# Kernel tuning notes

Measured on AMD Instinct MI355X. Metric: run time of the kernel, lower is better.

The kernel has to match this reference:

```python
import jax, jax.numpy as jnp
import numpy as np

# Fixed production-scale dims (equal-size graphs -> no ragged padding needed)
B, NPG, C, H, L, FFN, NC = 16, 512, 128, 8, 4, 512, 4
D = C // H          # head dim = 16
T = NPG + 1         # +1 virtual graph token
EPG = 8192          # edges per graph (avg degree 16)
E = B * EPG


def _ln(x, g, b, eps=1e-5):
    m = x.mean(-1, keepdims=True)
    v = ((x - m) ** 2).mean(-1, keepdims=True)
    return (x - m) * jax.lax.rsqrt(v + eps) * g + b


def setup_inputs() -> dict:
    key = jax.random.key(0)
    ks = jax.random.split(key, 24)
    N = B * NPG
    node_feats = jax.random.normal(ks[0], (N, 3), jnp.float32)
    # intra-graph edges: local endpoints + per-graph node offset (matches batch_ptr math)
    local = jax.random.randint(ks[1], (2, B, EPG), 0, NPG)
    offs = (jnp.arange(B) * NPG)[None, :, None]
    edge_index = (local + offs).reshape(2, E)
    edge_attr = jax.random.randint(ks[2], (E,), 0, 10)

    def nrm(k, shape, scale=0.02):
        return jax.random.normal(k, shape, jnp.float32) * scale

    params = {
        "W_node": nrm(ks[3], (3, C), 0.3), "b_node": jnp.zeros((C,), jnp.float32),
        "graph_token": nrm(ks[4], (C,), 1.0),
        "edge_bias_table": nrm(ks[5], (11, H), 0.1).at[0].set(0.0),  # padding_idx=0
        "in_deg_emb": nrm(ks[6], (512, C)).at[0].set(0.0),           # padding_idx=0
        "out_deg_emb": nrm(ks[7], (512, C)).at[0].set(0.0),
        "vnode_bias": nrm(ks[8], (H,), 1.0),
        "Wq": nrm(ks[9], (L, C, C)), "bq": jnp.zeros((L, C), jnp.float32),
        "Wk": nrm(ks[10], (L, C, C)), "bk": jnp.zeros((L, C), jnp.float32),
        "Wv": nrm(ks[11], (L, C, C)), "bv": jnp.zeros((L, C), jnp.float32),
        "Wo": nrm(ks[12], (L, C, C)), "bo": jnp.zeros((L, C), jnp.float32),
        "ln1_g": jnp.ones((L, C), jnp.float32), "ln1_b": jnp.zeros((L, C), jnp.float32),
        "ln2_g": jnp.ones((L, C), jnp.float32), "ln2_b": jnp.zeros((L, C), jnp.float32),
        "W1": nrm(ks[13], (L, C, FFN)), "b1": jnp.zeros((L, FFN), jnp.float32),
        "W2": nrm(ks[14], (L, FFN, C)), "b2": jnp.zeros((L, C), jnp.float32),
        "normf_g": jnp.ones((C,), jnp.float32), "normf_b": jnp.zeros((C,), jnp.float32),
        "Wc1": nrm(ks[15], (C, C // 2)), "bc1": jnp.zeros((C // 2,), jnp.float32),
        "Wc2": nrm(ks[16], (C // 2, NC)), "bc2": jnp.zeros((NC,), jnp.float32),
    }
    return {"node_feats": node_feats, "edge_index": edge_index,
            "edge_attr": edge_attr, "num_graphs": B, **params}


def reference(node_feats, W_node, b_node, graph_token, edge_bias_table,
              in_deg_emb, out_deg_emb, vnode_bias,
              Wq, bq, Wk, bk, Wv, bv, Wo, bo,
              ln1_g, ln1_b, ln2_g, ln2_b, W1, b1, W2, b2,
              normf_g, normf_b, Wc1, bc1, Wc2, bc2,
              edge_index, edge_attr, num_graphs):
    N = node_feats.shape[0]
    npg = N // num_graphs
    t = npg + 1
    src, dst = edge_index[0], edge_index[1]
    # degree encoders (scatter_add of ones == segment_sum)
    in_deg = jnp.clip(jax.ops.segment_sum(jnp.ones_like(dst), dst, num_segments=N), 0, 511)
    out_deg = jnp.clip(jax.ops.segment_sum(jnp.ones_like(src), src, num_segments=N), 0, 511)
    x_enc = node_feats @ W_node + b_node + in_deg_emb[in_deg] + out_deg_emb[out_deg]
    # equal-size graphs with sorted batch ids -> padding loop is a reshape, mask all-False
    x = jnp.concatenate(
        [jnp.broadcast_to(graph_token, (num_graphs, 1, C)),
         x_enc.reshape(num_graphs, npg, C)], axis=1)  # [B, T, C]
    # attention bias: vnode row/col + scattered edge-attr embeddings
    bias = jnp.zeros((num_graphs, H, t, t), jnp.float32)
    bias = bias.at[:, :, 0, :].set(vnode_bias[None, :, None])
    bias = bias.at[:, :, :, 0].set(vnode_bias[None, :, None])
    eb = edge_bias_table[jnp.clip(edge_attr, 0, 9) + 1]  # [E, H]
    g = src // npg
    sl = src - g * npg + 1
    dl = dst - g * npg + 1
    bias = bias.at[g, :, sl, dl].add(eb)  # duplicate edges accumulate (scatter_add)
    scale = 1.0 / np.sqrt(D).astype(np.float32)
    for l in range(L):  # key_padding_mask is all-False here -> masked_fill is a no-op
        h = _ln(x, ln1_g[l], ln1_b[l])
        q = (h @ Wq[l] + bq[l]).reshape(num_graphs, t, H, D)
        k = (h @ Wk[l] + bk[l]).reshape(num_graphs, t, H, D)
        v = (h @ Wv[l] + bv[l]).reshape(num_graphs, t, H, D)
        scores = jnp.einsum('bthd,bshd->bhts', q, k) * scale + bias
        attn = jax.nn.softmax(scores, axis=-1)
        o = jnp.einsum('bhts,bshd->bthd', attn, v).reshape(num_graphs, t, C)
        x = x + o @ Wo[l] + bo[l]
        h2 = _ln(x, ln2_g[l], ln2_b[l])
        x = x + jax.nn.gelu(h2 @ W1[l] + b1[l], approximate=False) @ W2[l] + b2[l]
    x = _ln(x, normf_g, normf_b)
    gr = x[:, 0, :]  # virtual-node readout
    return jax.nn.gelu(gr @ Wc1 + bc1, approximate=False) @ Wc2 + bc2
```

## Files before the change

kernel.cpp:

```cpp
#include <hip/hip_runtime.h>
#include <hip/hip_bf16.h>

#define BB 16
#define NPG 512
#define CC 128
#define HH 8
#define LL 4
#define FFN 512
#define NCLS 4
#define DD 16
#define TT 513
#define EE 131072
#define NNODES 8192
#define ROWS (BB * TT)
#define ECAP 64
#define SP 544
#define ESTR 68

static constexpr size_t XROWS = (size_t)BB * TT;
static constexpr size_t XSZ   = XROWS * CC;
static constexpr size_t VTSZ  = (size_t)BB * HH * DD * SP;

typedef unsigned short ushort_t;
typedef __attribute__((ext_vector_type(8))) short short8;
typedef __attribute__((ext_vector_type(4))) float floatx4;

__device__ __forceinline__ float gelu_exact(float v) {
    return 0.5f * v * (1.0f + erff(v * 0.70710678118654752440f));
}
__device__ __forceinline__ ushort_t f2bf(float f) {
    union { float f; unsigned u; } c; c.f = f;
    unsigned u = c.u;
    return (ushort_t)((u + 0x7FFFu + ((u >> 16) & 1u)) >> 16);
}
__device__ __forceinline__ int swz(int row, int col, int stride) {
    int kb = col >> 3;
    return row * stride + (((kb ^ (row & 7)) << 3) | (col & 7));
}

__device__ __forceinline__ void qkv_stage8(const ushort_t* hs,
                                           const ushort_t* Wtq, const float* bq_,
                                           const ushort_t* Wtk, const float* bk_,
                                           const ushort_t* Wtv, const float* bv_,
                                           ushort_t* qb, ushort_t* kb, ushort_t* vt,
                                           int b, int t0, int wave, int lq, int quad) {
    const short* hsS = (const short*)hs;
    int c = wave * 16 + lq;
    const short* Ws[3] = {(const short*)Wtq, (const short*)Wtk, (const short*)Wtv};
    const float* bs[3] = {bq_, bk_, bv_};
    size_t rB = (size_t)c * CC;

    #pragma unroll
    for (int m = 0; m < 3; ++m) {
        const short* W = Ws[m];
        floatx4 a0 = {0.f,0.f,0.f,0.f};
        #pragma unroll
        for (int k0 = 0; k0 < CC; k0 += 32) {
            short8 af = *(const short8*)(hsS + swz(lq, k0 + quad * 8, 128));
            short8 b0 = *(const short8*)(W + rB + k0 + quad * 8);
            a0 = __builtin_amdgcn_mfma_f32_16x16x32_bf16(af, b0, a0, 0, 0, 0);
        }
        float bv0 = bs[m][c];
        #pragma unroll
        for (int rg = 0; rg < 4; ++rg) {
            int t = t0 + quad * 4 + rg;
            if (t >= TT) continue;
            size_t r = (size_t)b * TT + t;
            float v0 = a0[rg] + bv0;
            if (m == 0) {
                qb[r * CC + c] = f2bf(v0 * 0.25f);
            } else if (m == 1) {
                kb[r * CC + c] = f2bf(v0);
            } else {
                vt[((size_t)(b * HH + wave) * DD + lq) * SP + t] = f2bf(v0);
            }
        }
    }
}

__global__ __launch_bounds__(256) void deg_csr_tr_kernel(const int* __restrict__ ei,
                                                         const int* __restrict__ ea,
                                                         int* __restrict__ deg_in,
                                                         int* __restrict__ deg_out,
                                                         int* __restrict__ cnt,
                                                         int* __restrict__ ebuf,
                                                         const float* __restrict__ Wq,
                                                         const float* __restrict__ Wk,
                                                         const float* __restrict__ Wv,
                                                         const float* __restrict__ Wo,
                                                         const float* __restrict__ W1,
                                                         const float* __restrict__ W2,
                                                         ushort_t* __restrict__ wtqkvo,
                                                         ushort_t* __restrict__ wt1,
                                                         ushort_t* __restrict__ wt2) {
    int bid = blockIdx.x;
    int tid = threadIdx.x;
    if (bid < 512) {
        int e = bid * 256 + tid;
        int src = ei[e], dst = ei[EE + e];
        atomicAdd(&deg_out[src], 1);
        atomicAdd(&deg_in[dst], 1);
        int g = src >> 9;
        int sl = src - (g << 9) + 1;
        int dl = dst - (g << 9) + 1;
        int a = ea[e];
        a = (a < 0) ? 0 : (a > 9 ? 9 : a);
        a += 1;
        int row = g * TT + sl;
        int pos = atomicAdd(&cnt[row], 1);
        if (pos < ECAP) ebuf[(size_t)row * ECAP + pos] = dl | (a << 16);
        return;
    }
    int z = bid - 512;
    const float* src; ushort_t* dst; int K, N, tile;
    if (z < 64) {
        int zz = z >> 2; tile = z & 3;
        int k = zz >> 2, l = zz & 3;
        const float* s4[4] = {Wq, Wk, Wv, Wo};
        src = s4[k] + (size_t)l * CC * CC;
        dst = wtqkvo + (size_t)(k * 4 + l) * 16384;
        K = CC; N = CC;
    } else if (z < 128) {
        int l = (z - 64) >> 4; tile = (z - 64) & 15;
        src = W1 + (size_t)l * CC * FFN;
        dst = wt1 + (size_t)l * 65536;
        K = CC; N = FFN;
    } else {
        int l = (z - 128) >> 4; tile = (z - 128) & 15;
        src = W2 + (size_t)l * FFN * CC;
        dst = wt2 + (size_t)l * 65536;
        K = FFN; N = CC;
    }
    int tilesN = N >> 6;
    int k0 = (tile / tilesN) << 6;
    int n0 = (tile - (tile / tilesN) * tilesN) << 6;
    __shared__ float t[64][65];
    int c = tid & 63, rb = tid >> 6;
    #pragma unroll
    for (int kk = 0; kk < 64; kk += 4)
        t[kk + rb][c] = src[(size_t)(k0 + kk + rb) * N + n0 + c];
    __syncthreads();
    #pragma unroll
    for (int nn = 0; nn < 64; nn += 4)
        dst[(size_t)(n0 + nn + rb) * K + k0 + c] = f2bf(t[c][nn + rb]);
}

__global__ __launch_bounds__(512) void pre_kernel(const float* __restrict__ nf,
                                                  const float* __restrict__ Wn,
                                                  const float* __restrict__ bn,
                                                  const float* __restrict__ gt,
                                                  const float* __restrict__ ide,
                                                  const float* __restrict__ ode,
                                                  const int* __restrict__ deg_in,
                                                  const int* __restrict__ deg_out,
                                                  const float* __restrict__ ln1g_,
                                                  const float* __restrict__ ln1b_,
                                                  const ushort_t* __restrict__ wtqkvo,
                                                  const float* __restrict__ bq_,
                                                  const float* __restrict__ bk_,
                                                  const float* __restrict__ bv_,
                                                  float* __restrict__ x_,
                                                  ushort_t* __restrict__ qb,
                                                  ushort_t* __restrict__ kb,
                                                  ushort_t* __restrict__ vt) {
    int bid = blockIdx.x;
    int tid = threadIdx.x;
    int b = bid / 33, qt = bid - b * 33;
    int t0 = qt * 16;
    int wave = tid >> 6, lane = tid & 63, lq = lane & 15, quad = lane >> 4;

    __shared__ ushort_t hs[16 * 128];
    __shared__ float sred[8][16][2];

    int c = wave * 16 + lq;
    float w0[4];
    #pragma unroll
    for (int rg = 0; rg < 4; ++rg) {
        int t = t0 + quad * 4 + rg;
        int tc = min(t, TT - 1);
        float v0;
        if (tc == 0) {
            v0 = gt[c];
        } else {
            int i = b * NPG + tc - 1;
            float f0 = nf[i*3+0], f1 = nf[i*3+1], f2 = nf[i*3+2];
            v0 = bn[c] + f0*Wn[0*CC + c] + f1*Wn[1*CC + c] + f2*Wn[2*CC + c];
            int di = min(deg_in[i], 511);
            int dq = min(deg_out[i], 511);
            v0 += ide[(size_t)di * CC + c] + ode[(size_t)dq * CC + c];
        }
        if (t < TT) x_[((size_t)b * TT + t) * CC + c] = v0;
        w0[rg] = v0;
    }
    #pragma unroll
    for (int rg = 0; rg < 4; ++rg) {
        float s1 = w0[rg];
        float s2 = w0[rg] * w0[rg];
        #pragma unroll
        for (int m = 1; m < 16; m <<= 1) {
            s1 += __shfl_xor(s1, m, 64);
            s2 += __shfl_xor(s2, m, 64);
        }
        if (lq == 0) { sred[wave][quad*4+rg][0] = s1; sred[wave][quad*4+rg][1] = s2; }
    }
    __syncthreads();
    float g0 = ln1g_[c], lb0 = ln1b_[c];
    #pragma unroll
    for (int rg = 0; rg < 4; ++rg) {
        int row = quad * 4 + rg;
        float S1 = 0.f, S2 = 0.f;
        #pragma unroll
        for (int w = 0; w < 8; ++w) { S1 += sred[w][row][0]; S2 += sred[w][row][1]; }
        float mn = S1 * (1.0f/CC);
        float var = S2 * (1.0f/CC) - mn * mn;
        float rs = rsqrtf(var + 1e-5f);
        hs[swz(row, c, 128)] = f2bf((w0[rg] - mn) * rs * g0 + lb0);
    }
    __syncthreads();
    qkv_stage8(hs, wtqkvo, bq_,
               wtqkvo + (size_t)4 * 16384, bk_,
               wtqkvo + (size_t)8 * 16384, bv_,
               qb, kb, vt, b, t0, wave, lq, quad);
}

__global__ __launch_bounds__(512, 4) void layer_kernel(const ushort_t* __restrict__ qbr,
                                                       const ushort_t* __restrict__ kbr,
                                                       const ushort_t* __restrict__ vtr,
                                                       const int* __restrict__ cnt,
                                                       const int* __restrict__ ebuf,
                                                       const float* __restrict__ ebt,
                                                       const float* __restrict__ vnode,
                                                       const ushort_t* __restrict__ WtO,
                                                       const float* __restrict__ bo_,
                                                       const float* __restrict__ ln2g_,
                                                       const float* __restrict__ ln2b_,
                                                       const ushort_t* __restrict__ Wt1_,
                                                       const float* __restrict__ b1_,
                                                       const ushort_t* __restrict__ Wt2_,
                                                       const float* __restrict__ b2_,
                                                       const float* __restrict__ ln1g_,
                                                       const float* __restrict__ ln1b_,
                                                       const ushort_t* __restrict__ Wtq,
                                                       const float* __restrict__ bq_,
                                                       const ushort_t* __restrict__ Wtk,
                                                       const float* __restrict__ bk_,
                                                       const ushort_t* __restrict__ Wtv,
                                                       const float* __restrict__ bv_,
                                                       const float* __restrict__ nfg,
                                                       const float* __restrict__ nfb,
                                                       const float* __restrict__ Wc1,
                                                       const float* __restrict__ bc1,
                                                       const float* __restrict__ Wc2,
                                                       const float* __restrict__ bc2,
                                                       float* __restrict__ x_,
                                                       ushort_t* __restrict__ qbw,
                                                       ushort_t* __restrict__ kbw,
                                                       ushort_t* __restrict__ vtw,
                                                       float* __restrict__ out,
                                                       int doQKV) {
    int qt = blockIdx.x, b = blockIdx.y;
    int tid = threadIdx.x;
    int wave = tid >> 6, lane = tid & 63, lq = lane & 15, quad = lane >> 4;

    __shared__ __align__(16) char arena[40960];
    float* strips = (float*)arena;
    int*   elist  = (int*)(arena + 34816);
    float* ebt_s  = (float*)(arena + 34816 + 4352);
    ushort_t* hs = (ushort_t*)arena;
    ushort_t* ms = (ushort_t*)(arena + 4096);
    __shared__ __align__(16) ushort_t obs[16 * 128];
    __shared__ float sred[8][16][2];
    __shared__ int cn_s[16];

    {
        int r = tid >> 5, j2 = (tid & 31) * 2;
        int qrow = qt * 16 + r;
        bool rv = (qrow >= 1) && (qrow < TT);
        size_t crow = (size_t)b * TT + (rv ? qrow : 0);
        if ((tid & 31) == 0) cn_s[r] = rv ? min(cnt[crow], ECAP) : 0;
        int2 ee = *(const int2*)(ebuf + crow * ECAP + j2);
        elist[r * ESTR + j2]     = ee.x;
        elist[r * ESTR + j2 + 1] = ee.y;
        if (tid < 88) ebt_s[tid] = ebt[tid];
    }
    __syncthreads();

    {
        int h = wave;
        int qg = qt * 16 + lq;
        int qr = min(qg, TT - 1);
        short8 z8 = {0,0,0,0,0,0,0,0};
        short8 qf = z8;
        if (quad < 2)
            qf = *(const short8*)(qbr + ((size_t)(b * TT + qr)) * CC + h * DD + quad * 8);
        float vn = vnode[h];
        const short* kbS = (const short*)kbr;
        const short* vtS = (const short*)(vtr + (size_t)(b * HH + h) * DD * SP);
        float* strip = strips + wave * (16 * ESTR);
        int cn = cn_s[lq];

        short8 af0c = z8, af1c = z8, vfc;
        {
            int kr0 = min(b * TT + lq, (int)XROWS - 1);
            int kr1 = min(b * TT + 16 + lq, (int)XROWS - 1);
            if (quad < 2) {
                af0c = *(const short8*)(kbS + (size_t)kr0 * CC + h * DD + quad * 8);
                af1c = *(const short8*)(kbS + (size_t)kr1 * CC + h * DD + quad * 8);
            }
            vfc = *(const short8*)(vtS + (size_t)lq * SP + quad * 8);
        }

        floatx4 oacc = {0.f, 0.f, 0.f, 0.f};
        float lsum = 0.f;

        for (int sp = 0; sp < 17; ++sp) {
            int spn = sp + 1;
            short8 af0n = z8, af1n = z8, vfn = z8;
            if (spn < 17) {
                int st0 = spn * 2, st1 = st0 + 1;
                int kr0 = min(b * TT + st0 * 16 + lq, (int)XROWS - 1);
                int kr1 = min(b * TT + st1 * 16 + lq, (int)XROWS - 1);
                if (quad < 2) {
                    af0n = *(const short8*)(kbS + (size_t)kr0 * CC + h * DD + quad * 8);
                    af1n = *(const short8*)(kbS + (size_t)kr1 * CC + h * DD + quad * 8);
                }
                vfn = *(const short8*)(vtS + (size_t)lq * SP + spn * 32 + quad * 8);
            }

            if (!(sp & 1)) {
                int w0 = sp * 32;
                #pragma unroll
                for (int k = 0; k < 5; ++k) {
                    int idx = lane + k * 64;
                    if (idx < 16 * ESTR / 4)
                        ((float4*)strip)[idx] = make_float4(0.f, 0.f, 0.f, 0.f);
                }
                asm volatile("s_waitcnt lgkmcnt(0)" ::: "memory");
                for (int j = quad; j < cn; j += 4) {
                    int e = elist[lq * ESTR + j];
                    int rel = (e & 0xFFFF) - w0;
                    if ((unsigned)rel < 64u)
                        atomicAdd(&strip[lq * ESTR + rel], ebt_s[(e >> 16) * 8 + h]);
                }
                asm volatile("s_waitcnt lgkmcnt(0)" ::: "memory");
            }

            float vadd = ((sp == 0) & (quad == 0) & (qg > 0)) ? vn : 0.f;
            int roff = lq * ESTR + (sp & 1) * 32 + quad * 4;
            float4 bia = *(const float4*)&strip[roff];
            float4 bib = *(const float4*)&strip[roff + 16];

            unsigned pw[2][2];
            #pragma unroll
            for (int t = 0; t < 2; ++t) {
                int st = sp * 2 + t;
                floatx4 cc4 = __builtin_amdgcn_mfma_f32_16x16x32_bf16(
                    t ? af1c : af0c, qf, (floatx4){0.f, 0.f, 0.f, 0.f}, 0, 0, 0);
                float4 bi = t ? bib : bia;
                float biv[4] = {bi.x, bi.y, bi.z, bi.w};
                float pr[4];
                #pragma unroll
                for (int rg = 0; rg < 4; ++rg) {
                    int s = st * 16 + quad * 4 + rg;
                    float bb = biv[rg];
                    if (t == 0 && rg == 0) bb += vadd;
                    float p = 0.f;
                    if (s < TT) p = __expf(cc4[rg] + bb);
                    lsum += p;
                    pr[rg] = p;
                }
                pw[t][0] = (unsigned)f2bf(pr[0]) | ((unsigned)f2bf(pr[1]) << 16);
                pw[t][1] = (unsigned)f2bf(pr[2]) | ((unsigned)f2bf(pr[3]) << 16);
            }
            int srcA = lq + (((2 * quad) & 3) << 4);
            int srcB = lq + (((2 * quad + 1) & 3) << 4);
            int a00 = __shfl((int)pw[0][0], srcA, 64);
            int a01 = __shfl((int)pw[0][1], srcA, 64);
            int a10 = __shfl((int)pw[1][0], srcA, 64);
            int a11 = __shfl((int)pw[1][1], srcA, 64);
            int b00 = __shfl((int)pw[0][0], srcB, 64);
            int b01 = __shfl((int)pw[0][1], srcB, 64);
            int b10 = __shfl((int)pw[1][0], srcB, 64);
            int b11 = __shfl((int)pw[1][1], srcB, 64);
            union { int u[4]; short8 s8; } pu;
            bool lo = quad < 2;
            pu.u[0] = lo ? a00 : a10;
            pu.u[1] = lo ? a01 : a11;
            pu.u[2] = lo ? b00 : b10;
            pu.u[3] = lo ? b01 : b11;
            oacc = __builtin_amdgcn_mfma_f32_16x16x32_bf16(vfc, pu.s8, oacc, 0, 0, 0);

            af0c = af0n; af1c = af1n; vfc = vfn;
        }

        lsum += __shfl_xor(lsum, 16, 64);
        lsum += __shfl_xor(lsum, 32, 64);
        #pragma unroll
        for (int rg = 0; rg < 4; ++rg)
            obs[swz(lq, h * DD + quad * 4 + rg, 128)] = f2bf(oacc[rg] / lsum);
    }
    __syncthreads();

    int t0 = qt * 16;
    int c = wave * 16 + lq;
    float vv0[4];
    const short* obsS = (const short*)obs;

    {
        const short* W = (const short*)WtO;
        size_t rB = (size_t)c * CC;
        floatx4 a0 = {0.f,0.f,0.f,0.f};
        #pragma unroll
        for (int k0 = 0; k0 < CC; k0 += 32) {
            short8 af = *(const short8*)(obsS + swz(lq, k0 + quad * 8, 128));
            short8 b0 = *(const short8*)(W + rB + k0 + quad * 8);
            a0 = __builtin_amdgcn_mfma_f32_16x16x32_bf16(af, b0, a0, 0, 0, 0);
        }
        float bv0 = bo_[c];
        #pragma unroll
        for (int rg = 0; rg < 4; ++rg) {
            int t = t0 + quad * 4 + rg;
            size_t rc = (size_t)b * TT + min(t, TT - 1);
            vv0[rg] = a0[rg] + bv0 + x_[rc * CC + c];
        }
        #pragma unroll
        for (int rg = 0; rg < 4; ++rg) {
            float s1 = vv0[rg];
            float s2 = vv0[rg] * vv0[rg];
            #pragma unroll
            for (int m = 1; m < 16; m <<= 1) {
                s1 += __shfl_xor(s1, m, 64);
                s2 += __shfl_xor(s2, m, 64);
            }
            if (lq == 0) { sred[wave][quad*4+rg][0] = s1; sred[wave][quad*4+rg][1] = s2; }
        }
        __syncthreads();
        float g0 = ln2g_[c], lb0 = ln2b_[c];
        #pragma unroll
        for (int rg = 0; rg < 4; ++rg) {
            int row = quad * 4 + rg;
            float S1 = 0.f, S2 = 0.f;
            #pragma unroll
            for (int w = 0; w < 8; ++w) { S1 += sred[w][row][0]; S2 += sred[w][row][1]; }
            float mn = S1 * (1.0f/CC);
            float var = S2 * (1.0f/CC) - mn * mn;
            float rs = rsqrtf(var + 1e-5f);
            hs[swz(row, c, 128)] = f2bf((vv0[rg] - mn) * rs * g0 + lb0);
        }
    }
    __syncthreads();

    {
        const short* hsS = (const short*)hs;
        const short* W = (const short*)Wt1_;
        #pragma unroll
        for (int nt = 0; nt < 4; ++nt) {
            int n = wave * 64 + nt * 16;
            size_t rB = (size_t)(n + lq) * CC;
            floatx4 a0 = {0.f,0.f,0.f,0.f};
            #pragma unroll
            for (int k0 = 0; k0 < CC; k0 += 32) {
                short8 af = *(const short8*)(hsS + swz(lq, k0 + quad * 8, 128));
                short8 b0 = *(const short8*)(W + rB + k0 + quad * 8);
                a0 = __builtin_amdgcn_mfma_f32_16x16x32_bf16(af, b0, a0, 0, 0, 0);
            }
            float bb0 = b1_[n + lq];
            #pragma unroll
            for (int rg = 0; rg < 4; ++rg)
                ms[swz(quad * 4 + rg, n + lq, 512)] = f2bf(gelu_exact(a0[rg] + bb0));
        }
    }
    __syncthreads();

    float w0[4];
    {
        const short* msS = (const short*)ms;
        const short* W = (const short*)Wt2_;
        size_t rB = (size_t)c * FFN;
        floatx4 a0 = {0.f,0.f,0.f,0.f};
        #pragma unroll 8
        for (int k0 = 0; k0 < FFN; k0 += 32) {
            short8 af = *(const short8*)(msS + swz(lq, k0 + quad * 8, 512));
            short8 b0 = *(const short8*)(W + rB + k0 + quad * 8);
            a0 = __builtin_amdgcn_mfma_f32_16x16x32_bf16(af, b0, a0, 0, 0, 0);
        }
        float bv0 = b2_[c];
        #pragma unroll
        for (int rg = 0; rg < 4; ++rg) {
            int t = t0 + quad * 4 + rg;
            w0[rg] = a0[rg] + bv0 + vv0[rg];
            if (t < TT) x_[((size_t)b * TT + t) * CC + c] = w0[rg];
        }
    }

    if (doQKV) {
        #pragma unroll
        for (int rg = 0; rg < 4; ++rg) {
            float s1 = w0[rg];
            float s2 = w0[rg] * w0[rg];
            #pragma unroll
            for (int m = 1; m < 16; m <<= 1) {
                s1 += __shfl_xor(s1, m, 64);
                s2 += __shfl_xor(s2, m, 64);
            }
            if (lq == 0) { sred[wave][quad*4+rg][0] = s1; sred[wave][quad*4+rg][1] = s2; }
        }
        __syncthreads();
        float g0 = ln1g_[c], lb0 = ln1b_[c];
        #pragma unroll
        for (int rg = 0; rg < 4; ++rg) {
            int row = quad * 4 + rg;
            float S1 = 0.f, S2 = 0.f;
            #pragma unroll
            for (int w = 0; w < 8; ++w) { S1 += sred[w][row][0]; S2 += sred[w][row][1]; }
            float mn = S1 * (1.0f/CC);
            float var = S2 * (1.0f/CC) - mn * mn;
            float rs = rsqrtf(var + 1e-5f);
            hs[swz(row, c, 128)] = f2bf((w0[rg] - mn) * rs * g0 + lb0);
        }
        __syncthreads();
        qkv_stage8(hs, Wtq, bq_, Wtk, bk_, Wtv, bv_, qbw, kbw, vtw, b, t0, wave, lq, quad);
        return;
    }

    if (qt != 0) return;

    __syncthreads();
    float* hrow = (float*)ms;
    float* xfs  = hrow + CC;
    float* c1s  = xfs + CC;
    float* red  = c1s + 64;
    if (quad == 0) hrow[c] = w0[0];
    __syncthreads();

    {
        int ct = tid;
        float v = 0.f, s1 = 0.f, s2 = 0.f;
        if (ct < CC) { v = hrow[ct]; s1 = v; s2 = v * v; }
        #pragma unroll
        for (int m = 32; m >= 1; m >>= 1) {
            s1 += __shfl_xor(s1, m, 64);
            s2 += __shfl_xor(s2, m, 64);
        }
        int w = ct >> 6;
        if (ct < CC && (ct & 63) == 0) { red[w*2] = s1; red[w*2+1] = s2; }
        __syncthreads();
        if (ct < CC) {
            float S1 = red[0] + red[2], S2 = red[1] + red[3];
            float mn = S1 * (1.0f/CC);
            float var = S2 * (1.0f/CC) - mn * mn;
            float rs = rsqrtf(var + 1e-5f);
            xfs[ct] = (v - mn) * rs * nfg[ct] + nfb[ct];
        }
        __syncthreads();
        if (ct < 64) {
            float acc = bc1[ct];
            #pragma unroll 4
            for (int k = 0; k < CC; ++k) acc = fmaf(xfs[k], Wc1[(size_t)k * 64 + ct], acc);
            c1s[ct] = gelu_exact(acc);
        }
        __syncthreads();
        if (ct < NCLS) {
            float acc = bc2[ct];
            #pragma unroll 4
            for (int j = 0; j < 64; ++j) acc = fmaf(c1s[j], Wc2[(size_t)j * NCLS + ct], acc);
            out[(size_t)b * NCLS + ct] = acc;
        }
    }
}

extern "C" void kernel_launch(void* const* d_in, const int* in_sizes, int n_in,
                              void* d_out, int out_size, void* d_ws, size_t ws_size,
                              hipStream_t stream) {
    const float* node_feats = (const float*)d_in[0];
    const int*   edge_index = (const int*)d_in[1];
    const int*   edge_attr  = (const int*)d_in[2];
    const float* W_node  = (const float*)d_in[4];
    const float* b_node  = (const float*)d_in[5];
    const float* g_token = (const float*)d_in[6];
    const float* ebt     = (const float*)d_in[7];
    const float* ide     = (const float*)d_in[8];
    const float* ode     = (const float*)d_in[9];
    const float* vnode   = (const float*)d_in[10];
    const float* Wq = (const float*)d_in[11];
    const float* bq = (const float*)d_in[12];
    const float* Wk = (const float*)d_in[13];
    const float* bk = (const float*)d_in[14];
    const float* Wv = (const float*)d_in[15];
    const float* bv = (const float*)d_in[16];
    const float* Wo = (const float*)d_in[17];
    const float* bo = (const float*)d_in[18];
    const float* ln1g = (const float*)d_in[19];
    const float* ln1b = (const float*)d_in[20];
    const float* ln2g = (const float*)d_in[21];
    const float* ln2b = (const float*)d_in[22];
    const float* W1 = (const float*)d_in[23];
    const float* b1 = (const float*)d_in[24];
    const float* W2 = (const float*)d_in[25];
    const float* b2 = (const float*)d_in[26];
    const float* nfg = (const float*)d_in[27];
    const float* nfb = (const float*)d_in[28];
    const float* Wc1 = (const float*)d_in[29];
    const float* bc1 = (const float*)d_in[30];
    const float* Wc2 = (const float*)d_in[31];
    const float* bc2 = (const float*)d_in[32];
    float* out = (float*)d_out;

    char* base = (char*)d_ws;
    float* x      = (float*)base;     base += XSZ * 4;
    ushort_t* qb0 = (ushort_t*)base;  base += XSZ * 2;
    ushort_t* kb0 = (ushort_t*)base;  base += XSZ * 2;
    ushort_t* vt0 = (ushort_t*)base;  base += VTSZ * 2;
    ushort_t* qb1 = (ushort_t*)base;  base += XSZ * 2;
    ushort_t* kb1 = (ushort_t*)base;  base += XSZ * 2;
    ushort_t* vt1 = (ushort_t*)base;  base += VTSZ * 2;
    ushort_t* wtqkvo = (ushort_t*)base; base += (size_t)16 * 16384 * 2;
    ushort_t* wt1 = (ushort_t*)base;  base += (size_t)4 * 65536 * 2;
    ushort_t* wt2 = (ushort_t*)base;  base += (size_t)4 * 65536 * 2;
    int* deg_in  = (int*)base;        base += NNODES * 4;
    int* deg_out = (int*)base;        base += NNODES * 4;
    int* cnt     = (int*)base;        base += (size_t)ROWS * 4;
    int* ebuf    = (int*)base;        base += (size_t)ROWS * ECAP * 4;

    ushort_t* qbs[2] = {qb0, qb1};
    ushort_t* kbs[2] = {kb0, kb1};
    ushort_t* vts[2] = {vt0, vt1};

    hipMemsetAsync(deg_in, 0, (size_t)(2 * NNODES + ROWS) * 4, stream);
    deg_csr_tr_kernel<<<512 + 192, 256, 0, stream>>>(
        edge_index, edge_attr, deg_in, deg_out, cnt, ebuf,
        Wq, Wk, Wv, Wo, W1, W2, wtqkvo, wt1, wt2);

    pre_kernel<<<528, 512, 0, stream>>>(
        node_feats, W_node, b_node, g_token, ide, ode, deg_in, deg_out,
        ln1g, ln1b, wtqkvo, bq, bk, bv, x, qb0, kb0, vt0);

    for (int l = 0; l < LL; ++l) {
        int rd = l & 1, wr = rd ^ 1;
        int ln = (l + 1) % LL;
        layer_kernel<<<dim3(33, BB), 512, 0, stream>>>(
            qbs[rd], kbs[rd], vts[rd], cnt, ebuf, ebt, vnode,
            wtqkvo + (size_t)(12 + l)*16384, bo + l*CC,
            ln2g + l*CC, ln2b + l*CC,
            wt1 + (size_t)l*65536, b1 + l*FFN,
            wt2 + (size_t)l*65536, b2 + l*CC,
            ln1g + ln*CC, ln1b + ln*CC,
            wtqkvo + (size_t)(0 + ln)*16384, bq + ln*CC,
            wtqkvo + (size_t)(4 + ln)*16384, bk + ln*CC,
            wtqkvo + (size_t)(8 + ln)*16384, bv + ln*CC,
            nfg, nfb, Wc1, bc1, Wc2, bc2,
            x, qbs[wr], kbs[wr], vts[wr], out,
            (l < LL-1) ? 1 : 0);
    }
}
```

Before: 465.0 us.

## Split fused layer kernel into per-head attention kernel and MLP kernel

```diff
diff --git a/kernel.cpp b/kernel.cpp
--- a/kernel.cpp
+++ b/kernel.cpp
@@ -15,7 +15,7 @@
 #define ROWS (BB * TT)
 #define ECAP 64
 #define SP 544
-#define ESTR 68
+#define SSTR 548
 
 static constexpr size_t XROWS = (size_t)BB * TT;
 static constexpr size_t XSZ   = XROWS * CC;
@@ -223,196 +223,209 @@
                qb, kb, vt, b, t0, wave, lq, quad);
 }
 
-__global__ __launch_bounds__(512, 4) void layer_kernel(const ushort_t* __restrict__ qbr,
-                                                       const ushort_t* __restrict__ kbr,
-                                                       const ushort_t* __restrict__ vtr,
-                                                       const int* __restrict__ cnt,
-                                                       const int* __restrict__ ebuf,
-                                                       const float* __restrict__ ebt,
-                                                       const float* __restrict__ vnode,
-                                                       const ushort_t* __restrict__ WtO,
-                                                       const float* __restrict__ bo_,
-                                                       const float* __restrict__ ln2g_,
-                                                       const float* __restrict__ ln2b_,
-                                                       const ushort_t* __restrict__ Wt1_,
-                                                       const float* __restrict__ b1_,
-                                                       const ushort_t* __restrict__ Wt2_,
-                                                       const float* __restrict__ b2_,
-                                                       const float* __restrict__ ln1g_,
-                                                       const float* __restrict__ ln1b_,
-                                                       const ushort_t* __restrict__ Wtq,
-                                                       const float* __restrict__ bq_,
-                                                       const ushort_t* __restrict__ Wtk,
-                                                       const float* __restrict__ bk_,
-                                                       const ushort_t* __restrict__ Wtv,
-                                                       const float* __restrict__ bv_,
-                                                       const float* __restrict__ nfg,
-                                                       const float* __restrict__ nfb,
-                                                       const float* __restrict__ Wc1,
-                                                       const float* __restrict__ bc1,
-                                                       const float* __restrict__ Wc2,
-                                                       const float* __restrict__ bc2,
-                                                       float* __restrict__ x_,
-                                                       ushort_t* __restrict__ qbw,
-                                                       ushort_t* __restrict__ kbw,
-                                                       ushort_t* __restrict__ vtw,
-                                                       float* __restrict__ out,
-                                                       int doQKV) {
+__global__ __launch_bounds__(256, 4) void attn_kernel(const ushort_t* __restrict__ qbr,
+                                                      const ushort_t* __restrict__ kbr,
+                                                      const ushort_t* __restrict__ vtr,
+                                                      const int* __restrict__ cnt,
+                                                      const int* __restrict__ ebuf,
+                                                      const float* __restrict__ ebt,
+                                                      const float* __restrict__ vnode,
+                                                      ushort_t* __restrict__ obf) {
+    int qt = blockIdx.x;
+    int bh = blockIdx.y;
+    int b = bh >> 3, h = bh & (HH - 1);
+    int tid = threadIdx.x;
+    int wave = tid >> 6, lane = tid & 63, lq = lane & 15, quad = lane >> 4;
+
+    __shared__ __align__(16) float strip[16 * SSTR];
+    __shared__ __align__(16) int elist[16 * 64];
+    __shared__ float ebtl[12];
+    __shared__ int cn_s[16];
+
+    for (int i = tid; i < 16 * SSTR / 4; i += 256)
+        ((float4*)strip)[i] = make_float4(0.f, 0.f, 0.f, 0.f);
+    if (tid < 11) ebtl[tid] = ebt[tid * 8 + h];
+    {
+        int r = tid >> 4, j4 = (tid & 15) * 4;
+        int qrow = qt * 16 + r;
+        bool rv = (qrow >= 1) && (qrow < TT);
+        size_t crow = (size_t)b * TT + (rv ? qrow : 0);
+        *(int4*)&elist[r * 64 + j4] = *(const int4*)(ebuf + crow * ECAP + j4);
+        if ((tid & 15) == 0) cn_s[r] = rv ? min(cnt[crow], ECAP) : 0;
+    }
+    __syncthreads();
+    if (tid < 16) {
+        int qrow = qt * 16 + tid;
+        if (qrow >= 1 && qrow < TT) strip[tid * SSTR] = vnode[h];
+    }
+    {
+        int r = tid >> 4;
+        int cn = cn_s[r];
+        for (int j = tid & 15; j < cn; j += 16) {
+            int e = elist[r * 64 + j];
+            atomicAdd(&strip[r * SSTR + (e & 0xFFFF)], ebtl[e >> 16]);
+        }
+    }
+    __syncthreads();
+
+    int qg = qt * 16 + lq;
+    int qr = min(qg, TT - 1);
+    short8 z8 = {0,0,0,0,0,0,0,0};
+    short8 qf = z8;
+    if (quad < 2)
+        qf = *(const short8*)(qbr + ((size_t)(b * TT + qr)) * CC + h * DD + quad * 8);
+    const short* kbS = (const short*)kbr;
+    const short* vtS = (const short*)(vtr + (size_t)bh * DD * SP);
+
+    floatx4 oacc = {0.f, 0.f, 0.f, 0.f};
+    float lsum = 0.f;
+
+    short8 af0c = z8, af1c = z8, vfc;
+    {
+        int sp = wave;
+        int st0 = sp * 2, st1 = st0 + 1;
+        int kr0 = min(b * TT + st0 * 16 + lq, (int)XROWS - 1);
+        int kr1 = min(b * TT + st1 * 16 + lq, (int)XROWS - 1);
+        if (quad < 2) {
+            af0c = *(const short8*)(kbS + (size_t)kr0 * CC + h * DD + quad * 8);
+            af1c = *(const short8*)(kbS + (size_t)kr1 * CC + h * DD + quad * 8);
+        }
+        vfc = *(const short8*)(vtS + (size_t)lq * SP + sp * 32 + quad * 8);
+    }
+
+    for (int sp = wave; sp < 17; sp += 4) {
+        int spn = sp + 4;
+        short8 af0n = z8, af1n = z8, vfn = z8;
+        if (spn < 17) {
+            int st0 = spn * 2, st1 = st0 + 1;
+            int kr0 = min(b * TT + st0 * 16 + lq, (int)XROWS - 1);
+            int kr1 = min(b * TT + st1 * 16 + lq, (int)XROWS - 1);
+            if (quad < 2) {
+                af0n = *(const short8*)(kbS + (size_t)kr0 * CC + h * DD + quad * 8);
+                af1n = *(const short8*)(kbS + (size_t)kr1 * CC + h * DD + quad * 8);
+            }
+            vfn = *(const short8*)(vtS + (size_t)lq * SP + spn * 32 + quad * 8);
+        }
+
+        int roff = lq * SSTR + sp * 32 + quad * 4;
+        float4 bia = *(const float4*)&strip[roff];
+        float4 bib = *(const float4*)&strip[roff + 16];
+
+        unsigned pw[2][2];
+        #pragma unroll
+        for (int t = 0; t < 2; ++t) {
+            int st = sp * 2 + t;
+            floatx4 cc4 = __builtin_amdgcn_mfma_f32_16x16x32_bf16(
+                t ? af1c : af0c, qf, (floatx4){0.f, 0.f, 0.f, 0.f}, 0, 0, 0);
+            float4 bi = t ? bib : bia;
+            float biv[4] = {bi.x, bi.y, bi.z, bi.w};
+            float pr[4];
+            #pragma unroll
+            for (int rg = 0; rg < 4; ++rg) {
+                int s = st * 16 + quad * 4 + rg;
+                float p = 0.f;
+                if (s < TT) p = __expf(cc4[rg] + biv[rg]);
+                lsum += p;
+                pr[rg] = p;
+            }
+            pw[t][0] = (unsigned)f2bf(pr[0]) | ((unsigned)f2bf(pr[1]) << 16);
+            pw[t][1] = (unsigned)f2bf(pr[2]) | ((unsigned)f2bf(pr[3]) << 16);
+        }
+        int srcA = lq + (((2 * quad) & 3) << 4);
+        int srcB = lq + (((2 * quad + 1) & 3) << 4);
+        int a00 = __shfl((int)pw[0][0], srcA, 64);
+        int a01 = __shfl((int)pw[0][1], srcA, 64);
+        int a10 = __shfl((int)pw[1][0], srcA, 64);
+        int a11 = __shfl((int)pw[1][1], srcA, 64);
+        int b00 = __shfl((int)pw[0][0], srcB, 64);
+        int b01 = __shfl((int)pw[0][1], srcB, 64);
+        int b10 = __shfl((int)pw[1][0], srcB, 64);
+        int b11 = __shfl((int)pw[1][1], srcB, 64);
+        union { int u[4]; short8 s8; } pu;
+        bool lo = quad < 2;
+        pu.u[0] = lo ? a00 : a10;
+        pu.u[1] = lo ? a01 : a11;
+        pu.u[2] = lo ? b00 : b10;
+        pu.u[3] = lo ? b01 : b11;
+        oacc = __builtin_amdgcn_mfma_f32_16x16x32_bf16(vfc, pu.s8, oacc, 0, 0, 0);
+
+        af0c = af0n; af1c = af1n; vfc = vfn;
+    }
+
+    lsum += __shfl_xor(lsum, 16, 64);
+    lsum += __shfl_xor(lsum, 32, 64);
+    __syncthreads();
+    float* redw = strip;
+    float* lsumS = strip + 1088;
+    #pragma unroll
+    for (int rg = 0; rg < 4; ++rg)
+        redw[wave * 272 + (quad * 4 + rg) * 17 + lq] = oacc[rg];
+    if (quad == 0) lsumS[wave * 16 + lq] = lsum;
+    __syncthreads();
+    {
+        int q = tid >> 4, d = tid & 15;
+        float o = 0.f, L = 0.f;
+        #pragma unroll
+        for (int w = 0; w < 4; ++w) {
+            o += redw[w * 272 + d * 17 + q];
+            L += lsumS[w * 16 + q];
+        }
+        int qq = qt * 16 + q;
+        if (qq < TT)
+            obf[((size_t)(b * TT + qq)) * CC + h * DD + d] = f2bf(o / L);
+    }
+}
+
+__global__ __launch_bounds__(512, 4) void mega_kernel(const ushort_t* __restrict__ obf,
+                                                      const ushort_t* __restrict__ WtO,
+                                                      const float* __restrict__ bo_,
+                                                      const float* __restrict__ ln2g_,
+                                                      const float* __restrict__ ln2b_,
+                                                      const ushort_t* __restrict__ Wt1_,
+                                                      const float* __restrict__ b1_,
+                                                      const ushort_t* __restrict__ Wt2_,
+                                                      const float* __restrict__ b2_,
+                                                      const float* __restrict__ ln1g_,
+                                                      const float* __restrict__ ln1b_,
+                                                      const ushort_t* __restrict__ Wtq,
+                                                      const float* __restrict__ bq_,
+                                                      const ushort_t* __restrict__ Wtk,
+                                                      const float* __restrict__ bk_,
+                                                      const ushort_t* __restrict__ Wtv,
+                                                      const float* __restrict__ bv_,
+                                                      const float* __restrict__ nfg,
+                                                      const float* __restrict__ nfb,
+                                                      const float* __restrict__ Wc1,
+                                                      const float* __restrict__ bc1,
+                                                      const float* __restrict__ Wc2,
+                                                      const float* __restrict__ bc2,
+                                                      float* __restrict__ x_,
+                                                      ushort_t* __restrict__ qbw,
+                                                      ushort_t* __restrict__ kbw,
+                                                      ushort_t* __restrict__ vtw,
+                                                      float* __restrict__ out,
+                                                      int doQKV) {
     int qt = blockIdx.x, b = blockIdx.y;
     int tid = threadIdx.x;
     int wave = tid >> 6, lane = tid & 63, lq = lane & 15, quad = lane >> 4;
 
-    __shared__ __align__(16) char arena[40960];
-    float* strips = (float*)arena;
-    int*   elist  = (int*)(arena + 34816);
-    float* ebt_s  = (float*)(arena + 34816 + 4352);
-    ushort_t* hs = (ushort_t*)arena;
-    ushort_t* ms = (ushort_t*)(arena + 4096);
-    __shared__ __align__(16) ushort_t obs[16 * 128];
+    __shared__ __align__(16) ushort_t hs[16 * 128];
+    __shared__ __align__(16) ushort_t ms[16 * 512];
     __shared__ float sred[8][16][2];
-    __shared__ int cn_s[16];
-
-    {
-        int r = tid >> 5, j2 = (tid & 31) * 2;
-        int qrow = qt * 16 + r;
-        bool rv = (qrow >= 1) && (qrow < TT);
-        size_t crow = (size_t)b * TT + (rv ? qrow : 0);
-        if ((tid & 31) == 0) cn_s[r] = rv ? min(cnt[crow], ECAP) : 0;
-        int2 ee = *(const int2*)(ebuf + crow * ECAP + j2);
-        elist[r * ESTR + j2]     = ee.x;
-        elist[r * ESTR + j2 + 1] = ee.y;
-        if (tid < 88) ebt_s[tid] = ebt[tid];
-    }
-    __syncthreads();
-
-    {
-        int h = wave;
-        int qg = qt * 16 + lq;
-        int qr = min(qg, TT - 1);
-        short8 z8 = {0,0,0,0,0,0,0,0};
-        short8 qf = z8;
-        if (quad < 2)
-            qf = *(const short8*)(qbr + ((size_t)(b * TT + qr)) * CC + h * DD + quad * 8);
-        float vn = vnode[h];
-        const short* kbS = (const short*)kbr;
-        const short* vtS = (const short*)(vtr + (size_t)(b * HH + h) * DD * SP);
-        float* strip = strips + wave * (16 * ESTR);
-        int cn = cn_s[lq];
-
-        short8 af0c = z8, af1c = z8, vfc;
-        {
-            int kr0 = min(b * TT + lq, (int)XROWS - 1);
-            int kr1 = min(b * TT + 16 + lq, (int)XROWS - 1);
-            if (quad < 2) {
-                af0c = *(const short8*)(kbS + (size_t)kr0 * CC + h * DD + quad * 8);
-                af1c = *(const short8*)(kbS + (size_t)kr1 * CC + h * DD + quad * 8);
-            }
-            vfc = *(const short8*)(vtS + (size_t)lq * SP + quad * 8);
-        }
-
-        floatx4 oacc = {0.f, 0.f, 0.f, 0.f};
-        float lsum = 0.f;
-
-        for (int sp = 0; sp < 17; ++sp) {
-            int spn = sp + 1;
-            short8 af0n = z8, af1n = z8, vfn = z8;
-            if (spn < 17) {
-                int st0 = spn * 2, st1 = st0 + 1;
-                int kr0 = min(b * TT + st0 * 16 + lq, (int)XROWS - 1);
-                int kr1 = min(b * TT + st1 * 16 + lq, (int)XROWS - 1);
-                if (quad < 2) {
-                    af0n = *(const short8*)(kbS + (size_t)kr0 * CC + h * DD + quad * 8);
-                    af1n = *(const short8*)(kbS + (size_t)kr1 * CC + h * DD + quad * 8);
-                }
-                vfn = *(const short8*)(vtS + (size_t)lq * SP + spn * 32 + quad * 8);
-            }
-
-            if (!(sp & 1)) {
-                int w0 = sp * 32;
-                #pragma unroll
-                for (int k = 0; k < 5; ++k) {
-                    int idx = lane + k * 64;
-                    if (idx < 16 * ESTR / 4)
-                        ((float4*)strip)[idx] = make_float4(0.f, 0.f, 0.f, 0.f);
-                }
-                asm volatile("s_waitcnt lgkmcnt(0)" ::: "memory");
-                for (int j = quad; j < cn; j += 4) {
-                    int e = elist[lq * ESTR + j];
-                    int rel = (e & 0xFFFF) - w0;
-                    if ((unsigned)rel < 64u)
-                        atomicAdd(&strip[lq * ESTR + rel], ebt_s[(e >> 16) * 8 + h]);
-                }
-                asm volatile("s_waitcnt lgkmcnt(0)" ::: "memory");
-            }
-
-            float vadd = ((sp == 0) & (quad == 0) & (qg > 0)) ? vn : 0.f;
-            int roff = lq * ESTR + (sp & 1) * 32 + quad * 4;
-            float4 bia = *(const float4*)&strip[roff];
-            float4 bib = *(const float4*)&strip[roff + 16];
-
-            unsigned pw[2][2];
-            #pragma unroll
-            for (int t = 0; t < 2; ++t) {
-                int st = sp * 2 + t;
-                floatx4 cc4 = __builtin_amdgcn_mfma_f32_16x16x32_bf16(
-                    t ? af1c : af0c, qf, (floatx4){0.f, 0.f, 0.f, 0.f}, 0, 0, 0);
-                float4 bi = t ? bib : bia;
-                float biv[4] = {bi.x, bi.y, bi.z, bi.w};
-                float pr[4];
-                #pragma unroll
-                for (int rg = 0; rg < 4; ++rg) {
-                    int s = st * 16 + quad * 4 + rg;
-                    float bb = biv[rg];
-                    if (t == 0 && rg == 0) bb += vadd;
-                    float p = 0.f;
-                    if (s < TT) p = __expf(cc4[rg] + bb);
-                    lsum += p;
-                    pr[rg] = p;
-                }
-                pw[t][0] = (unsigned)f2bf(pr[0]) | ((unsigned)f2bf(pr[1]) << 16);
-                pw[t][1] = (unsigned)f2bf(pr[2]) | ((unsigned)f2bf(pr[3]) << 16);
-            }
-            int srcA = lq + (((2 * quad) & 3) << 4);
-            int srcB = lq + (((2 * quad + 1) & 3) << 4);
-            int a00 = __shfl((int)pw[0][0], srcA, 64);
-            int a01 = __shfl((int)pw[0][1], srcA, 64);
-            int a10 = __shfl((int)pw[1][0], srcA, 64);
-            int a11 = __shfl((int)pw[1][1], srcA, 64);
-            int b00 = __shfl((int)pw[0][0], srcB, 64);
-            int b01 = __shfl((int)pw[0][1], srcB, 64);
-            int b10 = __shfl((int)pw[1][0], srcB, 64);
-            int b11 = __shfl((int)pw[1][1], srcB, 64);
-            union { int u[4]; short8 s8; } pu;
-            bool lo = quad < 2;
-            pu.u[0] = lo ? a00 : a10;
-            pu.u[1] = lo ? a01 : a11;
-            pu.u[2] = lo ? b00 : b10;
-            pu.u[3] = lo ? b01 : b11;
-            oacc = __builtin_amdgcn_mfma_f32_16x16x32_bf16(vfc, pu.s8, oacc, 0, 0, 0);
-
-            af0c = af0n; af1c = af1n; vfc = vfn;
-        }
-
-        lsum += __shfl_xor(lsum, 16, 64);
-        lsum += __shfl_xor(lsum, 32, 64);
-        #pragma unroll
-        for (int rg = 0; rg < 4; ++rg)
-            obs[swz(lq, h * DD + quad * 4 + rg, 128)] = f2bf(oacc[rg] / lsum);
-    }
-    __syncthreads();
 
     int t0 = qt * 16;
     int c = wave * 16 + lq;
     float vv0[4];
-    const short* obsS = (const short*)obs;
-
-    {
+
+    {
+        const short* obS = (const short*)obf;
+        size_t arow = (size_t)b * TT + min(t0 + lq, TT - 1);
         const short* W = (const short*)WtO;
         size_t rB = (size_t)c * CC;
         floatx4 a0 = {0.f,0.f,0.f,0.f};
         #pragma unroll
         for (int k0 = 0; k0 < CC; k0 += 32) {
-            short8 af = *(const short8*)(obsS + swz(lq, k0 + quad * 8, 128));
+            short8 af = *(const short8*)(obS + arow * CC + k0 + quad * 8);
             short8 b0 = *(const short8*)(W + rB + k0 + quad * 8);
             a0 = __builtin_amdgcn_mfma_f32_16x16x32_bf16(af, b0, a0, 0, 0, 0);
         }
@@ -614,6 +627,7 @@
     ushort_t* qb1 = (ushort_t*)base;  base += XSZ * 2;
     ushort_t* kb1 = (ushort_t*)base;  base += XSZ * 2;
     ushort_t* vt1 = (ushort_t*)base;  base += VTSZ * 2;
+    ushort_t* obf = (ushort_t*)base;  base += XSZ * 2;
     ushort_t* wtqkvo = (ushort_t*)base; base += (size_t)16 * 16384 * 2;
     ushort_t* wt1 = (ushort_t*)base;  base += (size_t)4 * 65536 * 2;
     ushort_t* wt2 = (ushort_t*)base;  base += (size_t)4 * 65536 * 2;
@@ -638,8 +652,12 @@
     for (int l = 0; l < LL; ++l) {
         int rd = l & 1, wr = rd ^ 1;
         int ln = (l + 1) % LL;
-        layer_kernel<<<dim3(33, BB), 512, 0, stream>>>(
-            qbs[rd], kbs[rd], vts[rd], cnt, ebuf, ebt, vnode,
+
+        attn_kernel<<<dim3(33, BB * HH), 256, 0, stream>>>(
+            qbs[rd], kbs[rd], vts[rd], cnt, ebuf, ebt, vnode, obf);
+
+        mega_kernel<<<dim3(33, BB), 512, 0, stream>>>(
+            obf,
             wtqkvo + (size_t)(12 + l)*16384, bo + l*CC,
             ln2g + l*CC, ln2b + l*CC,
             wt1 + (size_t)l*65536, b1 + l*FFN,
```

New measurement: 450.6 us. 3.1% less time.
